# Optimization experiments

Measured on AMD Instinct MI355X. Metric: run time of the kernel, lower is better.

## Reference

```python
import jax, jax.numpy as jnp
import numpy as np

EPS = 1e-5

def _ln(x, g, b):
    mu = jnp.mean(x, axis=-1, keepdims=True)
    var = jnp.mean(jnp.square(x - mu), axis=-1, keepdims=True)
    return (x - mu) * jax.lax.rsqrt(var + EPS) * g + b


def setup_inputs() -> dict:
    key = jax.random.key(0)
    ks = jax.random.split(key, 16)
    B, T, D, H = 8, 4096, 512, 1024
    s_d = 1.0 / np.sqrt(D)
    s_h = 1.0 / np.sqrt(H)
    return {
        "x": jax.random.normal(ks[0], (B, T, D), dtype=jnp.float32),
        "gamma": jnp.ones((D,), jnp.float32),
        "beta": jnp.zeros((D,), jnp.float32),
        "Wq": jax.random.uniform(ks[1], (D, H), jnp.float32, -s_d, s_d),
        "bq": jax.random.uniform(ks[2], (H,), jnp.float32, -s_d, s_d),
        "Wk": jax.random.uniform(ks[3], (D, H), jnp.float32, -s_d, s_d),
        "bk": jax.random.uniform(ks[4], (H,), jnp.float32, -s_d, s_d),
        "Wv": jax.random.uniform(ks[5], (D, H), jnp.float32, -s_d, s_d),
        "bv": jax.random.uniform(ks[6], (H,), jnp.float32, -s_d, s_d),
        "wbias": jax.random.uniform(ks[7], (H,), jnp.float32, 0.0, 1.0),
        "Wo": jax.random.uniform(ks[8], (H, D), jnp.float32, -s_h, s_h),
        "bo": jax.random.uniform(ks[9], (D,), jnp.float32, -s_h, s_h),
        "W1": jax.random.uniform(ks[10], (D, H), jnp.float32, -s_d, s_d),
        "b1": jax.random.uniform(ks[11], (H,), jnp.float32, -s_d, s_d),
        "W2": jax.random.uniform(ks[12], (H, D), jnp.float32, -s_h, s_h),
        "b2": jax.random.uniform(ks[13], (D,), jnp.float32, -s_h, s_h),
    }


def reference(x, gamma, beta, Wq, bq, Wk, bk, Wv, bv, wbias, Wo, bo, W1, b1, W2, b2):
    # --- pre-LN ---
    x1 = _ln(x, gamma, beta)                      # [B,T,D]
    # --- AFTFull attention (NOTE: sums over BATCH dim 0, as in original repo) ---
    Q = jnp.einsum('btd,dh->bth', x1, Wq) + bq    # [B,T,H]
    K = jnp.einsum('btd,dh->bth', x1, Wk) + bk
    V = jnp.einsum('btd,dh->bth', x1, Wv) + bv
    Q_sig = jax.nn.sigmoid(Q)
    numer = jnp.exp(K + wbias)                    # [B,T,H]
    denom = jnp.sum(numer, axis=0)                # [T,H]
    weighted = jnp.sum(numer * V, axis=0) / denom # [T,H]
    Yt = Q_sig * weighted                         # [B,T,H] (broadcast)
    Yt = jnp.einsum('bth,hd->btd', Yt, Wo) + bo   # [B,T,D]
    x2 = Yt + x1                                  # residual (dropout = identity, eval)
    # --- second LN (same params, as in original) + MLP ---
    x3 = _ln(x2, gamma, beta)
    h = jax.nn.gelu(jnp.einsum('btd,dh->bth', x3, W1) + b1, approximate=False)
    m = jnp.einsum('bth,hd->btd', h, W2) + b2
    # original: out = dropout(m) + m  ==  2*m at eval (no residual to x2)
    return m + m
```

## Files before the change

kernel.cpp:

```cpp
#include <hip/hip_runtime.h>
#include <hip/hip_bf16.h>
#include <cstdint>

using u16 = unsigned short;
using u32 = unsigned int;

typedef __bf16 bf16x8 __attribute__((ext_vector_type(8)));
typedef float  f32x4  __attribute__((ext_vector_type(4)));

#define DEV static __device__ __forceinline__

DEV float bf2f(u16 u){ union { u32 u; float f; } c; c.u = ((u32)u) << 16; return c.f; }

DEV u16 f2bf(float f){
  __bf16 h = (__bf16)f;
  return __builtin_bit_cast(u16, h);
}

DEV float fast_rcp(float x){ return __builtin_amdgcn_rcpf(x); }

DEV void async16(const u16* g, u16* l){
  __builtin_amdgcn_global_load_lds((const __attribute__((address_space(1))) u32*)g,
                                   (__attribute__((address_space(3))) u32*)l,
                                   16, 0, 0);
}

__global__ __launch_bounds__(256)
void transpose_to_bf16(const float* __restrict__ W, u16* __restrict__ WT, int R, int C){
  __shared__ float tile[32][33];
  const int c0 = blockIdx.x * 32, r0 = blockIdx.y * 32;
  const int tx = threadIdx.x, ty = threadIdx.y;
  #pragma unroll
  for (int j = 0; j < 4; ++j)
    tile[ty + j*8][tx] = W[(size_t)(r0 + ty + j*8) * C + (c0 + tx)];
  __syncthreads();
  #pragma unroll
  for (int j = 0; j < 4; ++j)
    WT[(size_t)(c0 + ty + j*8) * R + (r0 + tx)] = f2bf(tile[tx][ty + j*8]);
}

template<bool BF16IN>
__global__ __launch_bounds__(256)
void ln_kernel(const void* __restrict__ xin, const float* __restrict__ gamma,
               const float* __restrict__ beta, u16* __restrict__ xout){
  const int wid = threadIdx.x >> 6;
  const int lane = threadIdx.x & 63;
  const size_t row = (size_t)blockIdx.x * 4 + wid;
  const int d0 = lane * 8;
  float v[8];
  if constexpr (BF16IN){
    const u16* xp = (const u16*)xin + row * 512 + d0;
    uint4 p = *(const uint4*)xp;
    const u16* s = (const u16*)&p;
    #pragma unroll
    for (int i = 0; i < 8; ++i) v[i] = bf2f(s[i]);
  } else {
    const float* xp = (const float*)xin + row * 512 + d0;
    float4 p0 = *(const float4*)xp;
    float4 p1 = *(const float4*)(xp + 4);
    v[0]=p0.x; v[1]=p0.y; v[2]=p0.z; v[3]=p0.w;
    v[4]=p1.x; v[5]=p1.y; v[6]=p1.z; v[7]=p1.w;
  }
  float s = 0.f, sq = 0.f;
  #pragma unroll
  for (int i = 0; i < 8; ++i){ s += v[i]; sq += v[i]*v[i]; }
  #pragma unroll
  for (int o = 32; o >= 1; o >>= 1){ s += __shfl_xor(s, o); sq += __shfl_xor(sq, o); }
  const float mu  = s * (1.0f/512.0f);
  const float var = sq * (1.0f/512.0f) - mu*mu;
  const float rstd = rsqrtf(var + 1e-5f);
  u16 o8[8];
  #pragma unroll
  for (int i = 0; i < 8; ++i)
    o8[i] = f2bf((v[i]-mu)*rstd*gamma[d0+i] + beta[d0+i]);
  *(uint4*)(xout + row*512 + d0) = *(const uint4*)o8;
}

__global__ __launch_bounds__(256)
void aft_fused(const u16* __restrict__ numer, const u16* __restrict__ V,
               const u16* __restrict__ qs, u16* __restrict__ yt){
  const size_t TH = (size_t)4096 * 1024;
  const size_t i8 = ((size_t)blockIdx.x * 256 + threadIdx.x) * 8;
  float den[8], ws[8];
  #pragma unroll
  for (int j = 0; j < 8; ++j){ den[j] = 0.f; ws[j] = 0.f; }
  #pragma unroll
  for (int b = 0; b < 8; ++b){
    uint4 pn = *(const uint4*)(numer + b*TH + i8);
    uint4 pv = *(const uint4*)(V     + b*TH + i8);
    const u16* n = (const u16*)&pn;
    const u16* v = (const u16*)&pv;
    #pragma unroll
    for (int j = 0; j < 8; ++j){ float nf = bf2f(n[j]); den[j] += nf; ws[j] += nf * bf2f(v[j]); }
  }
  float w[8];
  #pragma unroll
  for (int j = 0; j < 8; ++j) w[j] = ws[j] * fast_rcp(den[j]);
  #pragma unroll
  for (int b = 0; b < 8; ++b){
    uint4 pq = *(const uint4*)(qs + b*TH + i8);
    const u16* q = (const u16*)&pq;
    u16 o[8];
    #pragma unroll
    for (int j = 0; j < 8; ++j) o[j] = f2bf(bf2f(q[j]) * w[j]);
    *(uint4*)(yt + b*TH + i8) = *(const uint4*)o;
  }
}

template<int EPI>
__global__ __launch_bounds__(256)
void gemm128(const u16* __restrict__ A, const u16* __restrict__ Bt, int K, int nTiles,
             const float* __restrict__ bias0, const float* __restrict__ bias1,
             const float* __restrict__ bias2, const float* __restrict__ wbias,
             u16* __restrict__ out0, u16* __restrict__ out1, u16* __restrict__ out2,
             const u16* __restrict__ resid, float* __restrict__ outf){
  __shared__ u16 ldsA[128*64];
  __shared__ u16 ldsB[128*64];
  const int tid  = threadIdx.x;
  const int wid  = tid >> 6;
  const int lane = tid & 63;
  const int quad = lane >> 4;
  const int lr   = lane & 15;

  const int lin = blockIdx.x;
  const int GS  = 16 * nTiles;
  const int g   = lin / GS;
  const int rem = lin - g * GS;
  const int tileM = (g * 16 + (rem & 15)) * 128;
  const int tileN = (rem >> 4) * 128;

  const int wmBase = (wid & 1) * 64;
  const int wnBase = (wid >> 1) * 64;

  const u16* Arow = A  + (size_t)tileM * K;
  const u16* Brow = Bt + (size_t)tileN * K;

  f32x4 acc[4][4] = {};

  int srow[4], scb[4];
  #pragma unroll
  for (int r = 0; r < 4; ++r){
    const int off = r*4096 + wid*1024 + lane*16;
    const int row = off >> 7;
    const int cbs = (off >> 4) & 7;
    srow[r] = row;
    scb[r]  = cbs ^ (row & 7);
  }

  for (int kt = 0; kt < K; kt += 64){
    #pragma unroll
    for (int r = 0; r < 4; ++r){
      const int ldsoff = r*4096 + wid*1024;
      async16(Arow + (size_t)srow[r]*K + kt + scb[r]*8, (u16*)((char*)ldsA + ldsoff));
      async16(Brow + (size_t)srow[r]*K + kt + scb[r]*8, (u16*)((char*)ldsB + ldsoff));
    }
    __syncthreads();
    #pragma unroll
    for (int s = 0; s < 2; ++s){
      bf16x8 ar[4], br[4];
      #pragma unroll
      for (int i = 0; i < 4; ++i){
        const int m = wmBase + i*16 + lr;
        const int cbs = (s*4 + quad) ^ (m & 7);
        ar[i] = *(const bf16x8*)((const char*)ldsA + m*128 + cbs*16);
      }
      #pragma unroll
      for (int i = 0; i < 4; ++i){
        const int n = wnBase + i*16 + lr;
        const int cbs = (s*4 + quad) ^ (n & 7);
        br[i] = *(const bf16x8*)((const char*)ldsB + n*128 + cbs*16);
      }
      #pragma unroll
      for (int i = 0; i < 4; ++i)
        #pragma unroll
        for (int j = 0; j < 4; ++j)
          acc[i][j] = __builtin_amdgcn_mfma_f32_16x16x32_bf16(br[j], ar[i], acc[i][j], 0, 0, 0);
    }
    __syncthreads();
  }

  if (EPI == 0){
    const int mat = tileN >> 10;
    const float* biasP = (mat==0) ? bias0 : (mat==1) ? bias1 : bias2;
    u16* outP          = (mat==0) ? out0  : (mat==1) ? out1  : out2;
    const int h0 = (tileN & 1023) + wnBase;
    #pragma unroll
    for (int j = 0; j < 4; ++j){
      const int colb = h0 + j*16 + quad*4;
      const float4 bvv = *(const float4*)(biasP + colb);
      float4 wbv = {0,0,0,0};
      if (mat == 1) wbv = *(const float4*)(wbias + colb);
      #pragma unroll
      for (int i = 0; i < 4; ++i){
        const int row = tileM + wmBase + i*16 + lr;
        u16 o[4];
        #pragma unroll
        for (int r = 0; r < 4; ++r){
          float v = acc[i][j][r] + ((const float*)&bvv)[r];
          if (mat == 0)      v = fast_rcp(1.0f + __expf(-v));
          else if (mat == 1) v = __expf(v + ((const float*)&wbv)[r]);
          o[r] = f2bf(v);
        }
        *(uint2*)(outP + (size_t)row * 1024 + colb) = *(const uint2*)o;
      }
    }
  } else if (EPI == 1){
    #pragma unroll
    for (int j = 0; j < 4; ++j){
      const int colb = tileN + wnBase + j*16 + quad*4;
      const float4 bvv = *(const float4*)(bias0 + colb);
      #pragma unroll
      for (int i = 0; i < 4; ++i){
        const int row = tileM + wmBase + i*16 + lr;
        uint2 pr = *(const uint2*)(resid + (size_t)row * 512 + colb);
        const u16* rp = (const u16*)&pr;
        u16 o[4];
        #pragma unroll
        for (int r = 0; r < 4; ++r)
          o[r] = f2bf(acc[i][j][r] + ((const float*)&bvv)[r] + bf2f(rp[r]));
        *(uint2*)(out0 + (size_t)row * 512 + colb) = *(const uint2*)o;
      }
    }
  } else if (EPI == 2){
    #pragma unroll
    for (int j = 0; j < 4; ++j){
      const int colb = tileN + wnBase + j*16 + quad*4;
      const float4 bvv = *(const float4*)(bias0 + colb);
      #pragma unroll
      for (int i = 0; i < 4; ++i){
        const int row = tileM + wmBase + i*16 + lr;
        u16 o[4];
        #pragma unroll
        for (int r = 0; r < 4; ++r){
          float v = acc[i][j][r] + ((const float*)&bvv)[r];
          float u2 = 2.0f * v * (0.7978845608f + 0.0356774081f * v * v);
          float t  = 1.0f - 2.0f * fast_rcp(1.0f + __expf(u2));
          o[r] = f2bf(0.5f * v * (1.0f + t));
        }
        *(uint2*)(out0 + (size_t)row * 1024 + colb) = *(const uint2*)o;
      }
    }
  } else {
    #pragma unroll
    for (int j = 0; j < 4; ++j){
      const int colb = tileN + wnBase + j*16 + quad*4;
      const float4 bvv = *(const float4*)(bias0 + colb);
      #pragma unroll
      for (int i = 0; i < 4; ++i){
        const int row = tileM + wmBase + i*16 + lr;
        float4 o;
        #pragma unroll
        for (int r = 0; r < 4; ++r)
          ((float*)&o)[r] = 2.0f * (acc[i][j][r] + ((const float*)&bvv)[r]);
        *(float4*)(outf + (size_t)row * 512 + colb) = o;
      }
    }
  }
}

extern "C" void kernel_launch(void* const* d_in, const int* in_sizes, int n_in,
                              void* d_out, int out_size, void* d_ws, size_t ws_size,
                              hipStream_t stream) {
  const float* x     = (const float*)d_in[0];
  const float* gamma = (const float*)d_in[1];
  const float* beta  = (const float*)d_in[2];
  const float* Wq    = (const float*)d_in[3];
  const float* bq    = (const float*)d_in[4];
  const float* Wk    = (const float*)d_in[5];
  const float* bk    = (const float*)d_in[6];
  const float* Wv    = (const float*)d_in[7];
  const float* bv    = (const float*)d_in[8];
  const float* wbias = (const float*)d_in[9];
  const float* Wo    = (const float*)d_in[10];
  const float* bo    = (const float*)d_in[11];
  const float* W1    = (const float*)d_in[12];
  const float* b1    = (const float*)d_in[13];
  const float* W2    = (const float*)d_in[14];
  const float* b2    = (const float*)d_in[15];
  float* out = (float*)d_out;

  char* w = (char*)d_ws;
  const size_t MB = 1ull << 20;
  u16* WqkvT = (u16*)(w + 0*MB);
  u16* WoT   = (u16*)(w + 3*MB);
  u16* W1T   = (u16*)(w + 4*MB);
  u16* W2T   = (u16*)(w + 5*MB);
  u16* x1b   = (u16*)(w + 6*MB);
  u16* Qs    = (u16*)(w + 38*MB);
  u16* Nu    = (u16*)(w + 102*MB);
  u16* Vb    = (u16*)(w + 166*MB);
  u16* Yt    = Nu;
  u16* x2b   = Vb;
  u16* x3b   = (u16*)(w + 198*MB);
  u16* hb    = Qs;

  dim3 tb(32, 8);
  transpose_to_bf16<<<dim3(32, 16), tb, 0, stream>>>(Wq, WqkvT,               512, 1024);
  transpose_to_bf16<<<dim3(32, 16), tb, 0, stream>>>(Wk, WqkvT + 1024*512,    512, 1024);
  transpose_to_bf16<<<dim3(32, 16), tb, 0, stream>>>(Wv, WqkvT + 2*1024*512,  512, 1024);
  transpose_to_bf16<<<dim3(16, 32), tb, 0, stream>>>(Wo, WoT, 1024, 512);
  transpose_to_bf16<<<dim3(32, 16), tb, 0, stream>>>(W1, W1T,  512, 1024);
  transpose_to_bf16<<<dim3(16, 32), tb, 0, stream>>>(W2, W2T, 1024, 512);

  ln_kernel<false><<<8192, 256, 0, stream>>>(x, gamma, beta, x1b);

  gemm128<0><<<256*24, 256, 0, stream>>>(x1b, WqkvT, 512, 24,
      bq, bk, bv, wbias, Qs, Nu, Vb, nullptr, nullptr);

  aft_fused<<<2048, 256, 0, stream>>>(Nu, Vb, Qs, Yt);

  gemm128<1><<<256*4, 256, 0, stream>>>(Yt, WoT, 1024, 4,
      bo, nullptr, nullptr, nullptr, x2b, nullptr, nullptr, x1b, nullptr);

  ln_kernel<true><<<8192, 256, 0, stream>>>(x2b, gamma, beta, x3b);

  gemm128<2><<<256*8, 256, 0, stream>>>(x3b, W1T, 512, 8,
      b1, nullptr, nullptr, nullptr, hb, nullptr, nullptr, nullptr, nullptr);

  gemm128<3><<<256*4, 256, 0, stream>>>(hb, W2T, 1024, 4,
      b2, nullptr, nullptr, nullptr, nullptr, nullptr, nullptr, nullptr, out);
}
```

Before: 501.5 us.

## Fuse AFT Q-sigmoid scaling into Wo GEMM A-load and merge weight transposes

The AFT kernel now writes only the batch-shared weighted tensor [T,H] instead of the full [B,T,H] Yt. The Wo GEMM multiplies Q_sig by that weight while staging A tiles into LDS, which removes a large write and re-read of Yt. The six weight-transpose launches are merged into a single 3D-grid launch. The GEMM also gets a compile-time K with a fully unrolled loop, precomputed LDS offsets and launch_bounds occupancy 3. The trade-off is that the A-operand path for the Wo GEMM becomes synchronous register loads instead of async LDS loads.

```diff
diff --git a/kernel.cpp b/kernel.cpp
--- a/kernel.cpp
+++ b/kernel.cpp
@@ -26,9 +26,24 @@
 }
 
 __global__ __launch_bounds__(256)
-void transpose_to_bf16(const float* __restrict__ W, u16* __restrict__ WT, int R, int C){
+void transpose_all(const float* __restrict__ W0, const float* __restrict__ W1,
+                   const float* __restrict__ W2, const float* __restrict__ W3,
+                   const float* __restrict__ W4, const float* __restrict__ W5,
+                   u16* __restrict__ T0, u16* __restrict__ T1, u16* __restrict__ T2,
+                   u16* __restrict__ T3, u16* __restrict__ T4, u16* __restrict__ T5){
+  const int z = blockIdx.z;
+  const float* W; u16* WT; int R, C;
+  switch (z){
+    case 0:  W = W0; WT = T0; R = 512;  C = 1024; break;
+    case 1:  W = W1; WT = T1; R = 512;  C = 1024; break;
+    case 2:  W = W2; WT = T2; R = 512;  C = 1024; break;
+    case 3:  W = W3; WT = T3; R = 1024; C = 512;  break;
+    case 4:  W = W4; WT = T4; R = 512;  C = 1024; break;
+    default: W = W5; WT = T5; R = 1024; C = 512;  break;
+  }
+  const int c0 = blockIdx.x * 32, r0 = blockIdx.y * 32;
+  if (c0 >= C || r0 >= R) return;
   __shared__ float tile[32][33];
-  const int c0 = blockIdx.x * 32, r0 = blockIdx.y * 32;
   const int tx = threadIdx.x, ty = threadIdx.y;
   #pragma unroll
   for (int j = 0; j < 4; ++j)
@@ -77,8 +92,8 @@
 }
 
 __global__ __launch_bounds__(256)
-void aft_fused(const u16* __restrict__ numer, const u16* __restrict__ V,
-               const u16* __restrict__ qs, u16* __restrict__ yt){
+void aft_weighted(const u16* __restrict__ numer, const u16* __restrict__ V,
+                  u16* __restrict__ wgt){
   const size_t TH = (size_t)4096 * 1024;
   const size_t i8 = ((size_t)blockIdx.x * 256 + threadIdx.x) * 8;
   float den[8], ws[8];
@@ -93,27 +108,20 @@
     #pragma unroll
     for (int j = 0; j < 8; ++j){ float nf = bf2f(n[j]); den[j] += nf; ws[j] += nf * bf2f(v[j]); }
   }
-  float w[8];
-  #pragma unroll
-  for (int j = 0; j < 8; ++j) w[j] = ws[j] * fast_rcp(den[j]);
-  #pragma unroll
-  for (int b = 0; b < 8; ++b){
-    uint4 pq = *(const uint4*)(qs + b*TH + i8);
-    const u16* q = (const u16*)&pq;
-    u16 o[8];
-    #pragma unroll
-    for (int j = 0; j < 8; ++j) o[j] = f2bf(bf2f(q[j]) * w[j]);
-    *(uint4*)(yt + b*TH + i8) = *(const uint4*)o;
-  }
-}
-
-template<int EPI>
-__global__ __launch_bounds__(256)
-void gemm128(const u16* __restrict__ A, const u16* __restrict__ Bt, int K, int nTiles,
-             const float* __restrict__ bias0, const float* __restrict__ bias1,
-             const float* __restrict__ bias2, const float* __restrict__ wbias,
+  u16 o[8];
+  #pragma unroll
+  for (int j = 0; j < 8; ++j) o[j] = f2bf(ws[j] * fast_rcp(den[j]));
+  *(uint4*)(wgt + i8) = *(const uint4*)o;
+}
+
+template<int EPI, int KC, bool AMUL>
+__global__ __launch_bounds__(256, 3)
+void gemm128(const u16* __restrict__ A, const u16* __restrict__ Bt, int nTiles,
+             const float* __restrict__ bias0, const float* __restrict__ wbias,
              u16* __restrict__ out0, u16* __restrict__ out1, u16* __restrict__ out2,
-             const u16* __restrict__ resid, float* __restrict__ outf){
+             const float* __restrict__ bias1, const float* __restrict__ bias2,
+             const u16* __restrict__ resid, float* __restrict__ outf,
+             const u16* __restrict__ wgt){
   __shared__ u16 ldsA[128*64];
   __shared__ u16 ldsB[128*64];
   const int tid  = threadIdx.x;
@@ -132,44 +140,65 @@
   const int wmBase = (wid & 1) * 64;
   const int wnBase = (wid >> 1) * 64;
 
-  const u16* Arow = A  + (size_t)tileM * K;
-  const u16* Brow = Bt + (size_t)tileN * K;
-
   f32x4 acc[4][4] = {};
 
   int srow[4], scb[4];
   #pragma unroll
   for (int r = 0; r < 4; ++r){
     const int off = r*4096 + wid*1024 + lane*16;
-    const int row = off >> 7;
-    const int cbs = (off >> 4) & 7;
-    srow[r] = row;
-    scb[r]  = cbs ^ (row & 7);
-  }
-
-  for (int kt = 0; kt < K; kt += 64){
-    #pragma unroll
-    for (int r = 0; r < 4; ++r){
-      const int ldsoff = r*4096 + wid*1024;
-      async16(Arow + (size_t)srow[r]*K + kt + scb[r]*8, (u16*)((char*)ldsA + ldsoff));
-      async16(Brow + (size_t)srow[r]*K + kt + scb[r]*8, (u16*)((char*)ldsB + ldsoff));
-    }
+    srow[r] = off >> 7;
+    scb[r]  = ((off >> 4) & 7) ^ (srow[r] & 7);
+  }
+  const u16* aSrc[4]; const u16* bSrc[4];
+  const u16* wSrc[4];
+  #pragma unroll
+  for (int r = 0; r < 4; ++r){
+    aSrc[r] = A  + (size_t)(tileM + srow[r]) * KC + scb[r]*8;
+    bSrc[r] = Bt + (size_t)(tileN + srow[r]) * KC + scb[r]*8;
+    if (AMUL) wSrc[r] = wgt + (size_t)((tileM + srow[r]) & 4095) * KC + scb[r]*8;
+  }
+
+  int aOff[2][4], bOff[2][4];
+  #pragma unroll
+  for (int s = 0; s < 2; ++s)
+    #pragma unroll
+    for (int i = 0; i < 4; ++i){
+      const int m = wmBase + i*16 + lr;
+      const int n = wnBase + i*16 + lr;
+      aOff[s][i] = m*128 + (((s*4 + quad) ^ (m & 7)) * 16);
+      bOff[s][i] = n*128 + (((s*4 + quad) ^ (n & 7)) * 16);
+    }
+
+  #pragma unroll
+  for (int kt = 0; kt < KC; kt += 64){
+    if constexpr (AMUL){
+      #pragma unroll
+      for (int r = 0; r < 4; ++r){
+        uint4 pq = *(const uint4*)(aSrc[r] + kt);
+        uint4 pw = *(const uint4*)(wSrc[r] + kt);
+        const u16* q = (const u16*)&pq;
+        const u16* wv = (const u16*)&pw;
+        u16 o[8];
+        #pragma unroll
+        for (int j = 0; j < 8; ++j) o[j] = f2bf(bf2f(q[j]) * bf2f(wv[j]));
+        *(uint4*)((char*)ldsA + r*4096 + wid*1024 + lane*16) = *(const uint4*)o;
+      }
+    } else {
+      #pragma unroll
+      for (int r = 0; r < 4; ++r)
+        async16(aSrc[r] + kt, (u16*)((char*)ldsA + r*4096 + wid*1024));
+    }
+    #pragma unroll
+    for (int r = 0; r < 4; ++r)
+      async16(bSrc[r] + kt, (u16*)((char*)ldsB + r*4096 + wid*1024));
     __syncthreads();
     #pragma unroll
     for (int s = 0; s < 2; ++s){
       bf16x8 ar[4], br[4];
       #pragma unroll
-      for (int i = 0; i < 4; ++i){
-        const int m = wmBase + i*16 + lr;
-        const int cbs = (s*4 + quad) ^ (m & 7);
-        ar[i] = *(const bf16x8*)((const char*)ldsA + m*128 + cbs*16);
-      }
-      #pragma unroll
-      for (int i = 0; i < 4; ++i){
-        const int n = wnBase + i*16 + lr;
-        const int cbs = (s*4 + quad) ^ (n & 7);
-        br[i] = *(const bf16x8*)((const char*)ldsB + n*128 + cbs*16);
-      }
+      for (int i = 0; i < 4; ++i) ar[i] = *(const bf16x8*)((const char*)ldsA + aOff[s][i]);
+      #pragma unroll
+      for (int i = 0; i < 4; ++i) br[i] = *(const bf16x8*)((const char*)ldsB + bOff[s][i]);
       #pragma unroll
       for (int i = 0; i < 4; ++i)
         #pragma unroll
@@ -289,34 +318,30 @@
   u16* Qs    = (u16*)(w + 38*MB);
   u16* Nu    = (u16*)(w + 102*MB);
   u16* Vb    = (u16*)(w + 166*MB);
-  u16* Yt    = Nu;
+  u16* Wgt   = (u16*)(w + 230*MB);
   u16* x2b   = Vb;
   u16* x3b   = (u16*)(w + 198*MB);
-  u16* hb    = Qs;
-
-  dim3 tb(32, 8);
-  transpose_to_bf16<<<dim3(32, 16), tb, 0, stream>>>(Wq, WqkvT,               512, 1024);
-  transpose_to_bf16<<<dim3(32, 16), tb, 0, stream>>>(Wk, WqkvT + 1024*512,    512, 1024);
-  transpose_to_bf16<<<dim3(32, 16), tb, 0, stream>>>(Wv, WqkvT + 2*1024*512,  512, 1024);
-  transpose_to_bf16<<<dim3(16, 32), tb, 0, stream>>>(Wo, WoT, 1024, 512);
-  transpose_to_bf16<<<dim3(32, 16), tb, 0, stream>>>(W1, W1T,  512, 1024);
-  transpose_to_bf16<<<dim3(16, 32), tb, 0, stream>>>(W2, W2T, 1024, 512);
+  u16* hb    = Nu;
+
+  transpose_all<<<dim3(32, 32, 6), dim3(32, 8), 0, stream>>>(
+      Wq, Wk, Wv, Wo, W1, W2,
+      WqkvT, WqkvT + 1024*512, WqkvT + 2*1024*512, WoT, W1T, W2T);
 
   ln_kernel<false><<<8192, 256, 0, stream>>>(x, gamma, beta, x1b);
 
-  gemm128<0><<<256*24, 256, 0, stream>>>(x1b, WqkvT, 512, 24,
-      bq, bk, bv, wbias, Qs, Nu, Vb, nullptr, nullptr);
-
-  aft_fused<<<2048, 256, 0, stream>>>(Nu, Vb, Qs, Yt);
-
-  gemm128<1><<<256*4, 256, 0, stream>>>(Yt, WoT, 1024, 4,
-      bo, nullptr, nullptr, nullptr, x2b, nullptr, nullptr, x1b, nullptr);
+  gemm128<0, 512, false><<<256*24, 256, 0, stream>>>(x1b, WqkvT, 24,
+      bq, wbias, Qs, Nu, Vb, bk, bv, nullptr, nullptr, nullptr);
+
+  aft_weighted<<<2048, 256, 0, stream>>>(Nu, Vb, Wgt);
+
+  gemm128<1, 1024, true><<<256*4, 256, 0, stream>>>(Qs, WoT, 4,
+      bo, nullptr, x2b, nullptr, nullptr, nullptr, nullptr, x1b, nullptr, Wgt);
 
   ln_kernel<true><<<8192, 256, 0, stream>>>(x2b, gamma, beta, x3b);
 
-  gemm128<2><<<256*8, 256, 0, stream>>>(x3b, W1T, 512, 8,
-      b1, nullptr, nullptr, nullptr, hb, nullptr, nullptr, nullptr, nullptr);
-
-  gemm128<3><<<256*4, 256, 0, stream>>>(hb, W2T, 1024, 4,
-      b2, nullptr, nullptr, nullptr, nullptr, nullptr, nullptr, nullptr, out);
-}
+  gemm128<2, 512, false><<<256*8, 256, 0, stream>>>(x3b, W1T, 8,
+      b1, nullptr, hb, nullptr, nullptr, nullptr, nullptr, nullptr, nullptr, nullptr);
+
+  gemm128<3, 1024, false><<<256*4, 256, 0, stream>>>(hb, W2T, 4,
+      b2, nullptr, nullptr, nullptr, nullptr, nullptr, nullptr, nullptr, out, nullptr);
+}
```

Result: slower. 513.8 us (+2.5%).
